# Performance work log

Hardware: AMD Instinct MI355X
Metric: run time of the kernel (lower is better)

The kernel has to match this reference:

```python
import jax, jax.numpy as jnp
import numpy as np

BN_EPS = 1e-3
NUM_HEADS = 4
HEAD_CH = 16  # embed_channels // num_heads = 64 // 4


def _conv_bn(x, w, g, b, rm, rv, pad):
    # Conv2d (no bias) followed by eval-mode BatchNorm2d, activation=Identity.
    y = jax.lax.conv_general_dilated(
        x, w, window_strides=(1, 1), padding=[(pad, pad), (pad, pad)],
        dimension_numbers=("NCHW", "OIHW", "NCHW"))
    s = g * jax.lax.rsqrt(rv + BN_EPS)
    return y * s[None, :, None, None] + (b - rm * s)[None, :, None, None]


def setup_inputs() -> dict:
    key = jax.random.key(0)
    ks = jax.random.split(key, 16)
    B, Cin, H, W = 8, 128, 160, 160
    N, Cg, Ce, Co = 80, 512, 64, 128
    x = jax.random.normal(ks[0], (B, Cin, H, W), jnp.float32)
    guide = jax.random.normal(ks[1], (B, N, Cg), jnp.float32)
    # embed_conv (1x1) + BN params
    w_embed = jax.random.normal(ks[2], (Ce, Cin, 1, 1), jnp.float32) * 0.05
    g1 = jnp.ones((Ce,), jnp.float32)
    b1 = jnp.zeros((Ce,), jnp.float32)
    rm1 = jax.random.normal(ks[3], (Ce,), jnp.float32) * 0.1
    rv1 = jax.random.uniform(ks[4], (Ce,), jnp.float32) + 0.5
    # guide_fc
    Wg = jax.random.normal(ks[5], (Ce, Cg), jnp.float32) * 0.02
    bg = jnp.zeros((Ce,), jnp.float32)
    # per-head bias
    attn_bias = jnp.zeros((NUM_HEADS,), jnp.float32)
    # project_conv (3x3) + BN params
    w_proj = jax.random.normal(ks[6], (Co, Cin, 3, 3), jnp.float32) * 0.02
    g2 = jnp.ones((Co,), jnp.float32)
    b2 = jnp.zeros((Co,), jnp.float32)
    rm2 = jax.random.normal(ks[7], (Co,), jnp.float32) * 0.1
    rv2 = jax.random.uniform(ks[8], (Co,), jnp.float32) + 0.5
    return {"x": x, "guide": guide, "w_embed": w_embed, "g1": g1, "b1": b1,
            "rm1": rm1, "rv1": rv1, "Wg": Wg, "bg": bg, "attn_bias": attn_bias,
            "w_proj": w_proj, "g2": g2, "b2": b2, "rm2": rm2, "rv2": rv2}


def reference(x, guide, w_embed, g1, b1, rm1, rv1, Wg, bg, attn_bias,
              w_proj, g2, b2, rm2, rv2):
    B, _, H, W = x.shape
    nh, hc = NUM_HEADS, HEAD_CH
    # guide_fc -> [B, N, nh, hc]
    g = (jnp.einsum("bnc,ec->bne", guide, Wg) + bg).reshape(B, -1, nh, hc)
    # embed_conv (1x1, BN, no act) -> [B, nh, hc, H, W]
    e = _conv_bn(x, w_embed, g1, b1, rm1, rv1, 0).reshape(B, nh, hc, H, W)
    # attn: dot over head channels, max over N guides, scale, bias, sigmoid
    aw = jnp.einsum("bmchw,bnmc->bmhwn", e, g)  # [B, nh, H, W, N]
    aw = jnp.max(aw, axis=-1) * (1.0 / np.sqrt(hc)) + attn_bias[None, :, None, None]
    aw = jax.nn.sigmoid(aw)  # scale == 1.0 (with_scale=False)
    # project_conv (3x3, BN, no act), gate per-head, merge heads
    xp = _conv_bn(x, w_proj, g2, b2, rm2, rv2, 1).reshape(B, nh, -1, H, W)
    return (xp * aw[:, :, None]).reshape(B, -1, H, W)
```

## Files before the change

kernel.cpp:

```cpp
#include <hip/hip_runtime.h>
#include <hip/hip_bf16.h>
#include <stdint.h>


typedef __attribute__((ext_vector_type(8))) short short8;
typedef __attribute__((ext_vector_type(4))) float f32x4;

#define PCH2 ((size_t)8 * 162 * 176 * 32)

#define GLDS(gp, lp) __builtin_amdgcn_global_load_lds(                         \
    (const __attribute__((address_space(1))) void*)(gp),                       \
    (__attribute__((address_space(3))) void*)(lp), 16, 0, 0)

__device__ __forceinline__ unsigned short f2bf(float f) {
  unsigned int u = __float_as_uint(f);
  u += 0x7fff + ((u >> 16) & 1);
  return (unsigned short)(u >> 16);
}

__global__ __launch_bounds__(256) void k_prep_x(const float* __restrict__ x,
                                                unsigned short* __restrict__ P2) {
  __shared__ unsigned short T[8192];
  int b = blockIdx.x / 112, blk = blockIdx.x % 112;
  int tid = threadIdx.x;
  int px = blk * 256 + tid;
  int hp = px / 176, wp = px - hp * 176;
  bool interior = (px < 28512) && (hp >= 1) && (hp <= 160) && (wp >= 8) && (wp < 168);
  const float* xb = x + (size_t)b * 128 * 25600 + (hp - 1) * 160 + (wp - 8);
  int q = tid >> 2, os = tid & 3;

  for (int cs = 0; cs < 4; ++cs) {
    short8 v[4];
#pragma unroll
    for (int s = 0; s < 4; ++s) {
#pragma unroll
      for (int j = 0; j < 8; ++j) {
        float f = interior ? xb[(size_t)(cs * 32 + s * 8 + j) * 25600] : 0.f;
        v[s][j] = (short)f2bf(f);
      }
    }
    if (cs) __syncthreads();
#pragma unroll
    for (int s = 0; s < 4; ++s)
      *(short8*)(&T[(tid * 4 + (s ^ (tid & 3))) * 8]) = v[s];
    __syncthreads();
#pragma unroll
    for (int ph = 0; ph < 4; ++ph) {
      int lpx = ph * 64 + q;
      int opx = blk * 256 + lpx;
      if (opx < 28512) {
        int ohp = opx / 176, owp = opx - ohp * 176;
        size_t obase = (((size_t)b * 162 + ohp) * 176 + owp) * 32 + os * 8;
        short8 w = *(const short8*)(&T[(lpx * 4 + (os ^ (lpx & 3))) * 8]);
        *(short8*)(&P2[(size_t)cs * PCH2 + obase]) = w;
      }
    }
  }
}

__global__ __launch_bounds__(256) void k_prep_misc(
    const float* __restrict__ w_embed, const float* __restrict__ w_proj,
    const float* __restrict__ g2, const float* __restrict__ b2,
    const float* __restrict__ rm2, const float* __restrict__ rv2,
    unsigned short* __restrict__ W1t, unsigned short* __restrict__ Wpt,
    float* __restrict__ s2, float* __restrict__ t2) {
  int idx = blockIdx.x * 256 + threadIdx.x;
  if (idx < 8192) { W1t[idx] = f2bf(w_embed[idx]); return; }
  idx -= 8192;
  if (idx < 147456) {
    int cs = idx / 36864, r = idx - cs * 36864;
    int tap = r >> 12, r2 = r & 4095;
    int co = r2 >> 5, ci5 = r2 & 31;
    int ci = cs * 32 + ci5;
    Wpt[idx] = f2bf(w_proj[(co * 128 + ci) * 9 + tap]);
    return;
  }
  idx -= 147456;
  if (idx < 128) {
    float s = g2[idx] * rsqrtf(rv2[idx] + 1e-3f);
    s2[idx] = s;
    t2[idx] = b2[idx] - rm2[idx] * s;
  }
}

__global__ __launch_bounds__(64) void k_guide(
    const float* __restrict__ guide, const float* __restrict__ Wg,
    const float* __restrict__ bg, const float* __restrict__ g1,
    const float* __restrict__ b1, const float* __restrict__ rm1,
    const float* __restrict__ rv1, unsigned short* __restrict__ Gpad,
    float* __restrict__ Cst) {
  int b = blockIdx.x / 80, n = blockIdx.x % 80;
  __shared__ float gs[512];
  const float* gr = guide + ((size_t)b * 80 + n) * 512;
  for (int i = threadIdx.x; i < 512; i += 64) gs[i] = gr[i];
  __syncthreads();
  int ce = threadIdx.x;
  const float* wr = Wg + (size_t)ce * 512;
  float acc = 0.f;
  for (int k = 0; k < 512; k += 4)
    acc += gs[k] * wr[k] + gs[k + 1] * wr[k + 1] + gs[k + 2] * wr[k + 2] +
           gs[k + 3] * wr[k + 3];
  float raw = acc + bg[ce];
  float s1 = g1[ce] * rsqrtf(rv1[ce] + 1e-3f);
  float t1 = b1[ce] - rm1[ce] * s1;
  int head = ce >> 4, c = ce & 15;
  size_t gp = (((size_t)b * 4 + head) * 80 + n) * 32;
  Gpad[gp + c] = f2bf(raw * s1);
  Gpad[gp + 16 + c] = 0;
  float cp = raw * t1;
  cp += __shfl_xor(cp, 1);
  cp += __shfl_xor(cp, 2);
  cp += __shfl_xor(cp, 4);
  cp += __shfl_xor(cp, 8);
  if (c == 0) Cst[((size_t)b * 4 + head) * 80 + n] = cp;
}

__global__ __launch_bounds__(256, 4) void k_mega(
    const unsigned short* __restrict__ P2, const unsigned short* __restrict__ W1t,
    const unsigned short* __restrict__ Wpt, const unsigned short* __restrict__ Gpad,
    const float* __restrict__ Cst, const float* __restrict__ attn_bias,
    const float* __restrict__ s2, const float* __restrict__ t2,
    float* __restrict__ out) {
  __shared__ unsigned short XA[2][7680];
  int b = blockIdx.x & 7;
  int r = blockIdx.x >> 3;
  int blkN = r & 1;
  int tile = r >> 1;
  int ht = tile / 5, wt = tile - ht * 5;
  int h0 = ht * 4, w0 = wt * 32;
  int tid = threadIdx.x, lane = tid & 63, wv = tid >> 6;
  int l15 = lane & 15, l4 = lane >> 4;
  int mh = wv >> 1, nh = wv & 1;

  size_t aoff[4];
#pragma unroll
  for (int k = 0; k < 4; ++k) {
    int i = wv * 4 + k;
    int c = i * 64 + lane;
    int cc = (c < 960) ? c : 0;
    int row = cc / 160, rem = cc - row * 160;
    int px = rem >> 2, sp = rem & 3;
    int s = sp ^ ((px >> 1) & 3);
    aoff[k] = (((size_t)b * 162 + h0 + row) * 176 + (w0 + 7 + px)) * 32 + s * 8;
  }
  int abase[2][3];
#pragma unroll
  for (int wh = 0; wh < 2; ++wh)
#pragma unroll
    for (int kx = 0; kx < 3; ++kx) {
      int px = wh * 16 + l15 + kx;
      abase[wh][kx] = px * 4 + (l4 ^ ((px >> 1) & 3));
    }
  int boff2[2];
#pragma unroll
  for (int nt = 0; nt < 2; ++nt)
    boff2[nt] = (blkN * 64 + nh * 32 + nt * 16 + l15) * 32 + l4 * 8;

  f32x4 acc[4][2], accE[4];
#pragma unroll
  for (int j = 0; j < 4; ++j) {
    acc[j][0] = (f32x4){0.f, 0.f, 0.f, 0.f};
    acc[j][1] = (f32x4){0.f, 0.f, 0.f, 0.f};
    accE[j]   = (f32x4){0.f, 0.f, 0.f, 0.f};
  }

#pragma unroll
  for (int k = 0; k < 4; ++k) {
    int i = wv * 4 + k;
    if (i < 15) GLDS(P2 + aoff[k], &XA[0][i * 512]);
  }
  short8 Bb[3][2];
#pragma unroll
  for (int nt = 0; nt < 2; ++nt) {
    Bb[0][nt] = *(const short8*)(Wpt + boff2[nt]);
    Bb[1][nt] = *(const short8*)(Wpt + 4096 + boff2[nt]);
  }
  __syncthreads();

#pragma unroll
  for (int cs = 0; cs < 4; ++cs) {
    if (cs < 3) {
#pragma unroll
      for (int k = 0; k < 4; ++k) {
        int i = wv * 4 + k;
        if (i < 15)
          GLDS(P2 + (size_t)(cs + 1) * PCH2 + aoff[k], &XA[(cs + 1) & 1][i * 512]);
      }
    }
#pragma unroll
    for (int tap = 0; tap < 9; ++tap) {
      const int t = cs * 9 + tap;
      if (t + 2 < 36) {
#pragma unroll
        for (int nt = 0; nt < 2; ++nt)
          Bb[(t + 2) % 3][nt] =
              *(const short8*)(Wpt + (size_t)(t + 2) * 4096 + boff2[nt]);
      }
      int ky = tap / 3, kx = tap - ky * 3;
      short8 A[4];
#pragma unroll
      for (int j = 0; j < 4; ++j) {
        int rr = mh * 2 + (j >> 1) + ky;
        A[j] = *(const short8*)(&XA[cs & 1][(rr * 160 + abase[j & 1][kx]) * 8]);
      }
      if (tap == 4) {
        short8 BE = *(const short8*)(W1t + (blkN * 32 + nh * 16 + l15) * 128 +
                                     cs * 32 + l4 * 8);
#pragma unroll
        for (int j = 0; j < 4; ++j)
          accE[j] = __builtin_amdgcn_mfma_f32_16x16x32_bf16(A[j], BE, accE[j], 0, 0, 0);
      }
#pragma unroll
      for (int j = 0; j < 4; ++j)
#pragma unroll
        for (int nt = 0; nt < 2; ++nt)
          acc[j][nt] = __builtin_amdgcn_mfma_f32_16x16x32_bf16(
              A[j], Bb[t % 3][nt], acc[j][nt], 0, 0, 0);
    }
    if (cs < 3) __syncthreads();
  }
  __syncthreads();

  unsigned short* Eb = &XA[0][0];
  float* AWLf = (float*)(&XA[0][0] + 4096);
#pragma unroll
  for (int j = 0; j < 4; ++j)
#pragma unroll
    for (int rr = 0; rr < 4; ++rr) {
      int pxl = (j >> 1) * 32 + (j & 1) * 16 + l4 * 4 + rr;
      int chunk = (l15 >> 3) ^ (pxl & 1);
      Eb[wv * 1024 + pxl * 16 + chunk * 8 + (l15 & 7)] = f2bf(accE[j][rr]);
    }

  const f32x4 zf = (f32x4){0.f, 0.f, 0.f, 0.f};
  int head = blkN * 2 + nh;
  short8 Ga[5];
  f32x4 cst[5];
#pragma unroll
  for (int m5 = 0; m5 < 5; ++m5) {
    Ga[m5] = *(const short8*)(Gpad + (((size_t)b * 4 + head) * 80 + m5 * 16 + l15) * 32 + l4 * 8);
    cst[m5] = *(const f32x4*)(Cst + ((size_t)b * 4 + head) * 80 + m5 * 16 + l4 * 4);
  }
  float bias = attn_bias[head];
#pragma unroll
  for (int nt = 0; nt < 4; ++nt) {
    int pxl = nt * 16 + l15;
    int chr = (l4 & 1) ^ (pxl & 1);
    short8 Bf = *(const short8*)(&Eb[wv * 1024 + pxl * 16 + chr * 8]);
    float mx = -3.0e38f;
#pragma unroll
    for (int m5 = 0; m5 < 5; ++m5) {
      f32x4 s = __builtin_amdgcn_mfma_f32_16x16x32_bf16(Ga[m5], Bf, zf, 0, 0, 0);
#pragma unroll
      for (int rr = 0; rr < 4; ++rr) mx = fmaxf(mx, s[rr] + cst[m5][rr]);
    }
    mx = fmaxf(mx, __shfl_xor(mx, 16));
    mx = fmaxf(mx, __shfl_xor(mx, 32));
    if (lane < 16) AWLf[wv * 64 + nt * 16 + lane] = 1.f / (1.f + __expf(-(mx * 0.25f + bias)));
  }

  float s2v[2], t2v[2];
#pragma unroll
  for (int nt = 0; nt < 2; ++nt) {
    int co = blkN * 64 + nh * 32 + nt * 16 + l15;
    s2v[nt] = s2[co];
    t2v[nt] = t2[co];
  }
#pragma unroll
  for (int j = 0; j < 4; ++j) {
    int h = h0 + mh * 2 + (j >> 1);
    int wbase = w0 + (j & 1) * 16 + l4 * 4;
    int pb = (j >> 1) * 32 + (j & 1) * 16 + l4 * 4;
    f32x4 a0 = *(const f32x4*)(&AWLf[wv * 64 + pb]);
#pragma unroll
    for (int nt = 0; nt < 2; ++nt) {
      int co = blkN * 64 + nh * 32 + nt * 16 + l15;
      f32x4 o;
#pragma unroll
      for (int rr = 0; rr < 4; ++rr) o[rr] = (acc[j][nt][rr] * s2v[nt] + t2v[nt]) * a0[rr];
      *(f32x4*)(out + (size_t)(b * 128 + co) * 25600 + h * 160 + wbase) = o;
    }
  }
}

extern "C" void kernel_launch(void* const* d_in, const int* in_sizes, int n_in,
                              void* d_out, int out_size, void* d_ws, size_t ws_size,
                              hipStream_t stream) {
  (void)in_sizes; (void)n_in; (void)out_size; (void)ws_size;
  const float* x         = (const float*)d_in[0];
  const float* guide     = (const float*)d_in[1];
  const float* w_embed   = (const float*)d_in[2];
  const float* g1        = (const float*)d_in[3];
  const float* b1        = (const float*)d_in[4];
  const float* rm1       = (const float*)d_in[5];
  const float* rv1       = (const float*)d_in[6];
  const float* Wg        = (const float*)d_in[7];
  const float* bg        = (const float*)d_in[8];
  const float* attn_bias = (const float*)d_in[9];
  const float* w_proj    = (const float*)d_in[10];
  const float* g2        = (const float*)d_in[11];
  const float* b2        = (const float*)d_in[12];
  const float* rm2       = (const float*)d_in[13];
  const float* rv2       = (const float*)d_in[14];
  float* out = (float*)d_out;

  char* ws = (char*)d_ws;
  unsigned short* P2   = (unsigned short*)(ws);
  unsigned short* W1t  = (unsigned short*)(ws + 58392576);
  unsigned short* Wpt  = (unsigned short*)(ws + 58408960);
  unsigned short* Gpad = (unsigned short*)(ws + 58703872);
  float* Cst           = (float*)(ws + 58867712);
  float* s2            = (float*)(ws + 58877952);
  float* t2            = (float*)(ws + 58878464);

  k_prep_x<<<8 * 112, 256, 0, stream>>>(x, P2);
  k_prep_misc<<<609, 256, 0, stream>>>(w_embed, w_proj, g2, b2, rm2, rv2, W1t, Wpt, s2, t2);
  k_guide<<<640, 64, 0, stream>>>(guide, Wg, bg, g1, b1, rm1, rv1, Gpad, Cst);
  k_mega<<<3200, 256, 0, stream>>>(P2, W1t, Wpt, Gpad, Cst, attn_bias, s2, t2, out);
}
```

Measured before the change: 171.6 us.

## Compute attention gate in a separate prologue phase before the 3x3 conv loop

The embed 1x1 conv, the guide dot-product max and the sigmoid gate are moved out of the main 3x3 conv loop into a separate phase at kernel start. That phase loads its own small center-pixel tile, writes the gate values to a dedicated shared array, and frees the embed accumulators before the big conv accumulation begins. The aim is to cut register pressure during the main loop and shorten the epilogue. In exchange it adds an extra round of global-to-LDS loads and four more barriers per block.

```diff
diff --git a/kernel.cpp b/kernel.cpp
--- a/kernel.cpp
+++ b/kernel.cpp
@@ -122,6 +122,7 @@
     const float* __restrict__ s2, const float* __restrict__ t2,
     float* __restrict__ out) {
   __shared__ unsigned short XA[2][7680];
+  __shared__ float AWL[4][64];
   int b = blockIdx.x & 7;
   int r = blockIdx.x >> 3;
   int blkN = r & 1;
@@ -132,6 +133,92 @@
   int l15 = lane & 15, l4 = lane >> 4;
   int mh = wv >> 1, nh = wv & 1;
 
+  {
+    int a2off[2];
+#pragma unroll
+    for (int k = 0; k < 2; ++k) {
+      int c = (wv * 2 + k) * 64 + lane;
+      int rr2 = c >> 7, rem = c & 127;
+      int p = rem >> 2, sp = rem & 3;
+      int s = sp ^ ((p >> 1) & 3);
+      a2off[k] = (int)(((b * 162 + h0 + 1 + rr2) * 176 + (w0 + 8 + p)) * 32 + s * 8);
+    }
+    int a2base[4];
+#pragma unroll
+    for (int j = 0; j < 4; ++j) {
+      int rr2 = mh * 2 + (j >> 1);
+      int p = (j & 1) * 16 + l15;
+      a2base[j] = rr2 * 128 + p * 4 + (l4 ^ ((p >> 1) & 3));
+    }
+
+    f32x4 accE[4];
+#pragma unroll
+    for (int j = 0; j < 4; ++j) accE[j] = (f32x4){0.f, 0.f, 0.f, 0.f};
+
+#pragma unroll
+    for (int k = 0; k < 2; ++k)
+      GLDS(P2 + a2off[k], &XA[0][(wv * 2 + k) * 512]);
+    __syncthreads();
+
+#pragma unroll
+    for (int cs = 0; cs < 4; ++cs) {
+      if (cs < 3) {
+#pragma unroll
+        for (int k = 0; k < 2; ++k)
+          GLDS(P2 + (size_t)(cs + 1) * PCH2 + a2off[k],
+               &XA[(cs + 1) & 1][(wv * 2 + k) * 512]);
+      }
+      short8 BE = *(const short8*)(W1t + (blkN * 32 + nh * 16 + l15) * 128 +
+                                   cs * 32 + l4 * 8);
+      short8 A2[4];
+#pragma unroll
+      for (int j = 0; j < 4; ++j)
+        A2[j] = *(const short8*)(&XA[cs & 1][a2base[j] * 8]);
+#pragma unroll
+      for (int j = 0; j < 4; ++j)
+        accE[j] = __builtin_amdgcn_mfma_f32_16x16x32_bf16(A2[j], BE, accE[j], 0, 0, 0);
+      __syncthreads();
+    }
+
+    unsigned short* Eb = &XA[0][0];
+#pragma unroll
+    for (int j = 0; j < 4; ++j)
+#pragma unroll
+      for (int rr = 0; rr < 4; ++rr) {
+        int pxl = (j >> 1) * 32 + (j & 1) * 16 + l4 * 4 + rr;
+        int chunk = (l15 >> 3) ^ (pxl & 1);
+        Eb[wv * 1024 + pxl * 16 + chunk * 8 + (l15 & 7)] = f2bf(accE[j][rr]);
+      }
+
+    const f32x4 zf = (f32x4){0.f, 0.f, 0.f, 0.f};
+    int head = blkN * 2 + nh;
+    short8 Ga[5];
+    f32x4 cst[5];
+#pragma unroll
+    for (int m5 = 0; m5 < 5; ++m5) {
+      Ga[m5] = *(const short8*)(Gpad + (((size_t)b * 4 + head) * 80 + m5 * 16 + l15) * 32 + l4 * 8);
+      cst[m5] = *(const f32x4*)(Cst + ((size_t)b * 4 + head) * 80 + m5 * 16 + l4 * 4);
+    }
+    float bias = attn_bias[head];
+#pragma unroll
+    for (int nt = 0; nt < 4; ++nt) {
+      int pxl = nt * 16 + l15;
+      int chr = (l4 & 1) ^ (pxl & 1);
+      short8 Bf = *(const short8*)(&Eb[wv * 1024 + pxl * 16 + chr * 8]);
+      float mx = -3.0e38f;
+#pragma unroll
+      for (int m5 = 0; m5 < 5; ++m5) {
+        f32x4 sc = __builtin_amdgcn_mfma_f32_16x16x32_bf16(Ga[m5], Bf, zf, 0, 0, 0);
+#pragma unroll
+        for (int rr = 0; rr < 4; ++rr) mx = fmaxf(mx, sc[rr] + cst[m5][rr]);
+      }
+      mx = fmaxf(mx, __shfl_xor(mx, 16));
+      mx = fmaxf(mx, __shfl_xor(mx, 32));
+      if (lane < 16) AWL[wv][nt * 16 + lane] = 1.f / (1.f + __expf(-(mx * 0.25f + bias)));
+    }
+  }
+  __syncthreads();
+
   size_t aoff[4];
 #pragma unroll
   for (int k = 0; k < 4; ++k) {
@@ -156,12 +243,11 @@
   for (int nt = 0; nt < 2; ++nt)
     boff2[nt] = (blkN * 64 + nh * 32 + nt * 16 + l15) * 32 + l4 * 8;
 
-  f32x4 acc[4][2], accE[4];
+  f32x4 acc[4][2];
 #pragma unroll
   for (int j = 0; j < 4; ++j) {
     acc[j][0] = (f32x4){0.f, 0.f, 0.f, 0.f};
     acc[j][1] = (f32x4){0.f, 0.f, 0.f, 0.f};
-    accE[j]   = (f32x4){0.f, 0.f, 0.f, 0.f};
   }
 
 #pragma unroll
@@ -203,13 +289,6 @@
         int rr = mh * 2 + (j >> 1) + ky;
         A[j] = *(const short8*)(&XA[cs & 1][(rr * 160 + abase[j & 1][kx]) * 8]);
       }
-      if (tap == 4) {
-        short8 BE = *(const short8*)(W1t + (blkN * 32 + nh * 16 + l15) * 128 +
-                                     cs * 32 + l4 * 8);
-#pragma unroll
-        for (int j = 0; j < 4; ++j)
-          accE[j] = __builtin_amdgcn_mfma_f32_16x16x32_bf16(A[j], BE, accE[j], 0, 0, 0);
-      }
 #pragma unroll
       for (int j = 0; j < 4; ++j)
 #pragma unroll
@@ -218,45 +297,6 @@
               A[j], Bb[t % 3][nt], acc[j][nt], 0, 0, 0);
     }
     if (cs < 3) __syncthreads();
-  }
-  __syncthreads();
-
-  unsigned short* Eb = &XA[0][0];
-  float* AWLf = (float*)(&XA[0][0] + 4096);
-#pragma unroll
-  for (int j = 0; j < 4; ++j)
-#pragma unroll
-    for (int rr = 0; rr < 4; ++rr) {
-      int pxl = (j >> 1) * 32 + (j & 1) * 16 + l4 * 4 + rr;
-      int chunk = (l15 >> 3) ^ (pxl & 1);
-      Eb[wv * 1024 + pxl * 16 + chunk * 8 + (l15 & 7)] = f2bf(accE[j][rr]);
-    }
-
-  const f32x4 zf = (f32x4){0.f, 0.f, 0.f, 0.f};
-  int head = blkN * 2 + nh;
-  short8 Ga[5];
-  f32x4 cst[5];
-#pragma unroll
-  for (int m5 = 0; m5 < 5; ++m5) {
-    Ga[m5] = *(const short8*)(Gpad + (((size_t)b * 4 + head) * 80 + m5 * 16 + l15) * 32 + l4 * 8);
-    cst[m5] = *(const f32x4*)(Cst + ((size_t)b * 4 + head) * 80 + m5 * 16 + l4 * 4);
-  }
-  float bias = attn_bias[head];
-#pragma unroll
-  for (int nt = 0; nt < 4; ++nt) {
-    int pxl = nt * 16 + l15;
-    int chr = (l4 & 1) ^ (pxl & 1);
-    short8 Bf = *(const short8*)(&Eb[wv * 1024 + pxl * 16 + chr * 8]);
-    float mx = -3.0e38f;
-#pragma unroll
-    for (int m5 = 0; m5 < 5; ++m5) {
-      f32x4 s = __builtin_amdgcn_mfma_f32_16x16x32_bf16(Ga[m5], Bf, zf, 0, 0, 0);
-#pragma unroll
-      for (int rr = 0; rr < 4; ++rr) mx = fmaxf(mx, s[rr] + cst[m5][rr]);
-    }
-    mx = fmaxf(mx, __shfl_xor(mx, 16));
-    mx = fmaxf(mx, __shfl_xor(mx, 32));
-    if (lane < 16) AWLf[wv * 64 + nt * 16 + lane] = 1.f / (1.f + __expf(-(mx * 0.25f + bias)));
   }
 
   float s2v[2], t2v[2];
@@ -271,7 +311,7 @@
     int h = h0 + mh * 2 + (j >> 1);
     int wbase = w0 + (j & 1) * 16 + l4 * 4;
     int pb = (j >> 1) * 32 + (j & 1) * 16 + l4 * 4;
-    f32x4 a0 = *(const f32x4*)(&AWLf[wv * 64 + pb]);
+    f32x4 a0 = *(const f32x4*)(&AWL[wv][pb]);
 #pragma unroll
     for (int nt = 0; nt < 2; ++nt) {
       int co = blkN * 64 + nh * 32 + nt * 16 + l15;
```

Result: faster. 142.9 us (-16.7%).
